# Optimization experiments

Hardware: AMD Instinct MI355X
Metric: run time of the kernel (lower is better)

## Reference

```python
import jax, jax.numpy as jnp
import numpy as np

EPS = 1e-5
TEMPERATURE = 1.0

def _finger_masks():
    # (5, 21) anatomical hyperedge masks: fingers cover node indices 1..20 in groups of 4
    m = np.zeros((5, 21), np.float32)
    for i in range(5):
        m[i, 1 + 4 * i: 5 + 4 * i] = 1.0
    return jnp.asarray(m)

def setup_inputs() -> dict:
    key = jax.random.key(0)
    ks = jax.random.split(key, 13)
    N, C, T, V, E = 128, 128, 256, 21, 8
    return {
        "x": jax.random.normal(ks[0], (N, C, T, V), jnp.float32),
        "dyn_w": jax.random.normal(ks[1], (E, C), jnp.float32) * 0.05,
        "dyn_b": jax.random.normal(ks[2], (E,), jnp.float32) * 0.05,
        "dyn_gamma": jax.random.uniform(ks[3], (E,), jnp.float32, 0.5, 1.5),
        "dyn_beta": jax.random.normal(ks[4], (E,), jnp.float32) * 0.05,
        "dyn_mean": jax.random.normal(ks[5], (E,), jnp.float32) * 0.05,
        "dyn_var": jax.random.uniform(ks[6], (E,), jnp.float32, 0.5, 1.5),
        "ft_w": jax.random.normal(ks[7], (C, C), jnp.float32) * 0.05,
        "ft_b": jax.random.normal(ks[8], (C,), jnp.float32) * 0.05,
        "ft_gamma": jax.random.uniform(ks[9], (C,), jnp.float32, 0.5, 1.5),
        "ft_beta": jax.random.normal(ks[10], (C,), jnp.float32) * 0.05,
        "ft_mean": jax.random.normal(ks[11], (C,), jnp.float32) * 0.05,
        "ft_var": jax.random.uniform(ks[12], (C,), jnp.float32, 0.5, 1.5),
    }

def reference(x, dyn_w, dyn_b, dyn_gamma, dyn_beta, dyn_mean, dyn_var,
              ft_w, ft_b, ft_gamma, ft_beta, ft_mean, ft_var):
    N = x.shape[0]
    # dynamic hyperedge generation: mean over T -> conv1x1 -> BN -> ReLU -> softmax over V
    xm = x.mean(axis=2)                                         # (N, C, V)
    h = jnp.einsum('ncv,ec->nev', xm, dyn_w) + dyn_b[None, :, None]
    scale = dyn_gamma * jax.lax.rsqrt(dyn_var + EPS)
    h = (h - dyn_mean[None, :, None]) * scale[None, :, None] + dyn_beta[None, :, None]
    h = jax.nn.relu(h)
    H_dyn = jax.nn.softmax(h / TEMPERATURE, axis=-1)            # (N, E, V)
    H_phy = jnp.broadcast_to(_finger_masks()[None], (N, 5, 21))
    H = jnp.concatenate([H_dyn, H_phy], axis=1)                 # (N, M=E+5, V)
    # feature transform: conv1x1 -> BN -> ReLU
    xf = jnp.einsum('nctv,oc->notv', x, ft_w) + ft_b[None, :, None, None]
    fscale = ft_gamma * jax.lax.rsqrt(ft_var + EPS)
    xf = (xf - ft_mean[None, :, None, None]) * fscale[None, :, None, None] + ft_beta[None, :, None, None]
    xf = jax.nn.relu(xf)                                        # (N, Cout, T, V)
    # hypergraph message passing: node -> edge -> node
    Y = jnp.einsum('nmv,nctv->ncmt', H, xf)                     # (N, Cout, M, T)
    Xr = jnp.einsum('nmv,ncmt->nctv', H, Y)                     # (N, Cout, T, V)
    return Xr + x  # residual (in_channels == out_channels)
```

## Files before the change

### kernel.cpp

```cpp
#include <hip/hip_runtime.h>
#include <hip/hip_bf16.h>
#include <math.h>

#define EPS 1e-5f

static constexpr int N_ = 128, C_ = 128, T_ = 256, V_ = 21, E_ = 8, M_ = 13;
static constexpr int TV_ = T_ * V_;
static constexpr int NT_ = 8;
static constexpr int ST_ = NT_ * V_;
static constexpr int XF_PITCH = 48;

typedef short bf16x8 __attribute__((ext_vector_type(8)));
typedef short s16x4  __attribute__((ext_vector_type(4)));
typedef float f32x4  __attribute__((ext_vector_type(4)));

__device__ inline short f2bf(float v) {
    __hip_bfloat16 b = __float2bfloat16(v);
    return *reinterpret_cast<short*>(&b);
}

__global__ __launch_bounds__(256) void prep_kernel(
    const float* __restrict__ ft_w, const float* __restrict__ ft_b,
    const float* __restrict__ ft_gamma, const float* __restrict__ ft_beta,
    const float* __restrict__ ft_mean, const float* __restrict__ ft_var,
    __hip_bfloat16* __restrict__ w_bf, float* __restrict__ sc_g, float* __restrict__ sh_g)
{
    int tid = blockIdx.x * 256 + threadIdx.x;
    if (tid < C_ * C_) w_bf[tid] = __float2bfloat16(ft_w[tid]);
    if (tid < C_) {
        float sc = ft_gamma[tid] * rsqrtf(ft_var[tid] + EPS);
        sc_g[tid] = sc;
        sh_g[tid] = (ft_b[tid] - ft_mean[tid]) * sc + ft_beta[tid];
    }
}

__global__ __launch_bounds__(256) void mean_kernel(const float* __restrict__ x,
                                                   float* __restrict__ xm) {
    __shared__ float slab[TV_];
    __shared__ float partial[V_ * 8];
    const int nc = blockIdx.x;
    const int tid = threadIdx.x;
    const float4* src4 = (const float4*)(x + (size_t)nc * TV_);
    float4* slab4 = (float4*)slab;
    #pragma unroll
    for (int it = 0; it < 6; ++it) {
        int idx = it * 256 + tid;
        if (idx < TV_ / 4) slab4[idx] = src4[idx];
    }
    __syncthreads();
    if (tid < V_ * 8) {
        int v = tid >> 3, g = tid & 7;
        float s = 0.f;
        #pragma unroll
        for (int tt = 0; tt < 32; ++tt) s += slab[(g * 32 + tt) * V_ + v];
        partial[v * 8 + g] = s;
    }
    __syncthreads();
    if (tid < V_) {
        float s = 0.f;
        #pragma unroll
        for (int g = 0; g < 8; ++g) s += partial[tid * 8 + g];
        xm[(size_t)nc * V_ + tid] = s * (1.0f / T_);
    }
}

__global__ __launch_bounds__(64) void hyper_kernel(
    const float* __restrict__ xm, const float* __restrict__ dyn_w,
    const float* __restrict__ dyn_b,
    const float* __restrict__ dyn_gamma, const float* __restrict__ dyn_beta,
    const float* __restrict__ dyn_mean, const float* __restrict__ dyn_var,
    __hip_bfloat16* __restrict__ A_bf)
{
    __shared__ float xs[C_ * V_];
    __shared__ float Hs[M_ * V_];
    const int n = blockIdx.x;
    const int l = threadIdx.x;
    const float* src = xm + (size_t)n * C_ * V_;
    for (int idx = l; idx < C_ * V_; idx += 64) xs[idx] = src[idx];
    __syncthreads();
    for (int idx = l; idx < E_ * V_; idx += 64) {
        int e = idx / V_, v = idx - e * V_;
        float acc = 0.f;
        for (int c = 0; c < C_; ++c) acc = fmaf(xs[c * V_ + v], dyn_w[e * C_ + c], acc);
        acc += dyn_b[e];
        float scale = dyn_gamma[e] * rsqrtf(dyn_var[e] + EPS);
        acc = (acc - dyn_mean[e]) * scale + dyn_beta[e];
        Hs[idx] = fmaxf(acc, 0.f);
    }
    __syncthreads();
    if (l < E_) {
        float row[V_];
        float mx = -1e30f;
        #pragma unroll
        for (int v = 0; v < V_; ++v) { row[v] = Hs[l * V_ + v]; mx = fmaxf(mx, row[v]); }
        float s = 0.f;
        #pragma unroll
        for (int v = 0; v < V_; ++v) { row[v] = __expf(row[v] - mx); s += row[v]; }
        float inv = 1.0f / s;
        #pragma unroll
        for (int v = 0; v < V_; ++v) Hs[l * V_ + v] = row[v] * inv;
    } else if (l < M_) {
        int i = l - E_;
        #pragma unroll
        for (int v = 0; v < V_; ++v)
            Hs[l * V_ + v] = (v >= 1 + 4 * i && v < 5 + 4 * i) ? 1.0f : 0.0f;
    }
    __syncthreads();
    for (int idx = l; idx < 32 * 32; idx += 64) {
        int u = idx >> 5, v = idx & 31;
        float s = 0.f;
        if (u < V_ && v < V_) {
            #pragma unroll
            for (int m = 0; m < M_; ++m) s = fmaf(Hs[m * V_ + u], Hs[m * V_ + v], s);
        }
        A_bf[(size_t)n * 1024 + idx] = __float2bfloat16(s);
    }
}

__global__ __launch_bounds__(512) void main_kernel(
    const float* __restrict__ x, const __hip_bfloat16* __restrict__ w_bf,
    const float* __restrict__ sc_g, const float* __restrict__ sh_g,
    const __hip_bfloat16* __restrict__ A_bf, float* __restrict__ out)
{
    __shared__ __align__(16) char lds[49280];
    __shared__ float sc_s[C_], sh_s[C_];

    const int st = blockIdx.x;
    const int n  = blockIdx.y;
    const int tid = threadIdx.x;
    const int w = tid >> 6;
    const int l = tid & 63;
    const int hi = l >> 4;
    const int lo = l & 15;
    const int s0 = st * ST_;
    const size_t xbase = (size_t)n * C_ * TV_ + s0;

    if (tid < C_) { sc_s[tid] = sc_g[tid]; sh_s[tid] = sh_g[tid]; }

    const int o_row = 16 * w + lo;
    bf16x8 wf[4];
    #pragma unroll
    for (int kk = 0; kk < 4; ++kk)
        wf[kk] = *(const bf16x8*)((const short*)w_bf + o_row * C_ + kk * 32 + 8 * hi);

    const short* Abf_n = (const short*)A_bf + (size_t)n * 1024;
    const bf16x8 bA0 = *(const bf16x8*)(Abf_n + lo * 32 + 8 * hi);
    const bf16x8 bA1 = *(const bf16x8*)(Abf_n + (16 + lo) * 32 + 8 * hi);

    for (int idx = tid; idx < (C_ / 4) * (ST_ / 4); idx += 512) {
        int cg = idx / (ST_ / 4), q = idx - cg * (ST_ / 4);
        int c0 = cg * 4, sq = q * 4;
        f32x4 f[4];
        #pragma unroll
        for (int i = 0; i < 4; ++i)
            f[i] = *(const f32x4*)(x + xbase + (size_t)(c0 + i) * TV_ + sq);
        #pragma unroll
        for (int i = 0; i < 4; ++i) {
            int s = sq + i;
            s16x4 pk;
            #pragma unroll
            for (int j = 0; j < 4; ++j) pk[j] = f2bf(f[j][i]);
            int byte = (s * 256 + c0 * 2) ^ ((s & 7) << 4);
            *(s16x4*)(lds + byte) = pk;
        }
    }
    if (tid < 256) {
        int s = ST_ + (tid >> 5);
        int c4 = (tid & 31) * 4;
        int byte = (s * 256 + c4 * 2) ^ ((s & 7) << 4);
        *(unsigned long long*)(lds + byte) = 0ull;
    }
    __syncthreads();

    f32x4 acc[11];
    #pragma unroll
    for (int nf = 0; nf < 11; ++nf) acc[nf] = (f32x4){0.f, 0.f, 0.f, 0.f};
    #pragma unroll
    for (int kk = 0; kk < 4; ++kk) {
        #pragma unroll
        for (int nf = 0; nf < 11; ++nf) {
            int srow = 16 * nf + lo;
            int byte = (srow * 256 + (kk * 32 + 8 * hi) * 2) ^ ((srow & 7) << 4);
            bf16x8 b = *(const bf16x8*)(lds + byte);
            acc[nf] = __builtin_amdgcn_mfma_f32_16x16x32_bf16(wf[kk], b, acc[nf], 0, 0, 0);
        }
    }
    __syncthreads();

    const int obase = 16 * w + 4 * hi;
    float scr[4], shr[4];
    #pragma unroll
    for (int r = 0; r < 4; ++r) { scr[r] = sc_s[obase + r]; shr[r] = sh_s[obase + r]; }
    #pragma unroll
    for (int nf = 0; nf < 11; ++nf) {
        int s = 16 * nf + lo;
        if (s < ST_) {
            int t = s / V_, u = s - t * V_;
            #pragma unroll
            for (int r = 0; r < 4; ++r) {
                float vv = fmaxf(fmaf(acc[nf][r], scr[r], shr[r]), 0.f);
                *(short*)(lds + ((obase + r) * 8 + t) * XF_PITCH + u * 2) = f2bf(vv);
            }
        }
    }
    for (int row = tid; row < 1024; row += 512) {
        *(short*)(lds + row * XF_PITCH + 42) = 0;
        *(int*)(lds + row * XF_PITCH + 44) = 0;
    }
    if (tid < 4) *(int*)(lds + 49152 + tid * 4) = 0;
    __syncthreads();

    bf16x8 xfr[8];
    #pragma unroll
    for (int i = 0; i < 8; ++i) {
        int row = 16 * (8 * w + i) + lo;
        xfr[i] = *(const bf16x8*)(lds + row * XF_PITCH + 16 * hi);
    }
    #pragma unroll
    for (int i = 0; i < 8; ++i) {
        f32x4 d0 = (f32x4){0.f, 0.f, 0.f, 0.f};
        f32x4 d1 = (f32x4){0.f, 0.f, 0.f, 0.f};
        d0 = __builtin_amdgcn_mfma_f32_16x16x32_bf16(xfr[i], bA0, d0, 0, 0, 0);
        d1 = __builtin_amdgcn_mfma_f32_16x16x32_bf16(xfr[i], bA1, d1, 0, 0, 0);
        int row0 = 16 * (8 * w + i) + 4 * hi;
        #pragma unroll
        for (int r = 0; r < 4; ++r) {
            int row = row0 + r;
            int o = row >> 3, t = row & 7;
            size_t g = xbase + (size_t)o * TV_ + t * V_;
            out[g + lo] = d0[r] + x[g + lo];
            if (lo < V_ - 16) out[g + 16 + lo] = d1[r] + x[g + 16 + lo];
        }
    }
}

extern "C" void kernel_launch(void* const* d_in, const int* in_sizes, int n_in,
                              void* d_out, int out_size, void* d_ws, size_t ws_size,
                              hipStream_t stream) {
    const float* x         = (const float*)d_in[0];
    const float* dyn_w     = (const float*)d_in[1];
    const float* dyn_b     = (const float*)d_in[2];
    const float* dyn_gamma = (const float*)d_in[3];
    const float* dyn_beta  = (const float*)d_in[4];
    const float* dyn_mean  = (const float*)d_in[5];
    const float* dyn_var   = (const float*)d_in[6];
    const float* ft_w      = (const float*)d_in[7];
    const float* ft_b      = (const float*)d_in[8];
    const float* ft_gamma  = (const float*)d_in[9];
    const float* ft_beta   = (const float*)d_in[10];
    const float* ft_mean   = (const float*)d_in[11];
    const float* ft_var    = (const float*)d_in[12];
    float* out = (float*)d_out;

    char* ws = (char*)d_ws;
    float* xm  = (float*)ws;                                   ws += (size_t)N_ * C_ * V_ * 4;
    __hip_bfloat16* A_bf = (__hip_bfloat16*)ws;                ws += (size_t)N_ * 1024 * 2;
    __hip_bfloat16* w_bf = (__hip_bfloat16*)ws;                ws += (size_t)C_ * C_ * 2;
    float* sc_g = (float*)ws;                                  ws += C_ * 4;
    float* sh_g = (float*)ws;                                  ws += C_ * 4;

    prep_kernel<<<64, 256, 0, stream>>>(ft_w, ft_b, ft_gamma, ft_beta, ft_mean, ft_var,
                                        w_bf, sc_g, sh_g);
    mean_kernel<<<N_ * C_, 256, 0, stream>>>(x, xm);
    hyper_kernel<<<N_, 64, 0, stream>>>(xm, dyn_w, dyn_b, dyn_gamma, dyn_beta,
                                        dyn_mean, dyn_var, A_bf);
    main_kernel<<<dim3(32, 128), 512, 0, stream>>>(x, w_bf, sc_g, sh_g, A_bf, out);
}
```

Baseline: 336.8 us.

## Pre-transpose x into bf16 MFMA fragment tiles fused with mean reduction

Adds a transpose kernel that reads x once, converts it to bf16 in MFMA-fragment order in a workspace buffer, and accumulates the T-mean with atomics. This replaces the separate mean pass over fp32 x. The main kernel then loads the pre-swizzled tiles straight into LDS with global_load_lds and takes the residual from the bf16 tile instead of re-reading fp32 x. The main kernel's second stage is split into two halves so LDS use drops and more blocks can run per CU. Trade-offs: a bf16 residual loses precision, the bf16 intermediate costs extra global writes and reads, and a sliced fallback path is used when the workspace is too small.

```diff
diff --git a/kernel.cpp b/kernel.cpp
--- a/kernel.cpp
+++ b/kernel.cpp
@@ -8,22 +8,35 @@
 static constexpr int TV_ = T_ * V_;
 static constexpr int NT_ = 8;
 static constexpr int ST_ = NT_ * V_;
-static constexpr int XF_PITCH = 48;
+static constexpr int TILE_B = 176 * 256;
+static constexpr int NCHUNK = TILE_B / 1024;
+static constexpr int SPITCH = 272;
+static constexpr int XFOFF = TILE_B;
+static constexpr int XF_BYTES = 512 * 48 + 64;
 
 typedef short bf16x8 __attribute__((ext_vector_type(8)));
 typedef short s16x4  __attribute__((ext_vector_type(4)));
 typedef float f32x4  __attribute__((ext_vector_type(4)));
 
-__device__ inline short f2bf(float v) {
-    __hip_bfloat16 b = __float2bfloat16(v);
-    return *reinterpret_cast<short*>(&b);
+__device__ inline short f2bf(float v) { __hip_bfloat16 b = __float2bfloat16(v); return *reinterpret_cast<short*>(&b); }
+__device__ inline float bf2f(short s) { __hip_bfloat16 b = *reinterpret_cast<__hip_bfloat16*>(&s); return __bfloat162float(b); }
+__device__ inline int saddr(int s, int c2) { return (s * SPITCH + c2) ^ (((s >> 2) & 7) << 4); }
+__device__ inline int fragb(int s, int c) {
+    return ((c >> 5) * 11 + (s >> 4)) * 1024 + (((c >> 3) & 3) * 16 + (s & 15)) * 16 + (c & 7) * 2;
+}
+#define EXOR(r) ((((r) >> 5) & 3) << 4)
+
+__device__ inline void gload16(const void* g, void* l) {
+    __builtin_amdgcn_global_load_lds((const __attribute__((address_space(1))) unsigned int*)g,
+                                     (__attribute__((address_space(3))) unsigned int*)l, 16, 0, 0);
 }
 
 __global__ __launch_bounds__(256) void prep_kernel(
     const float* __restrict__ ft_w, const float* __restrict__ ft_b,
     const float* __restrict__ ft_gamma, const float* __restrict__ ft_beta,
     const float* __restrict__ ft_mean, const float* __restrict__ ft_var,
-    __hip_bfloat16* __restrict__ w_bf, float* __restrict__ sc_g, float* __restrict__ sh_g)
+    __hip_bfloat16* __restrict__ w_bf, float* __restrict__ sc_g, float* __restrict__ sh_g,
+    float* __restrict__ xm)
 {
     int tid = blockIdx.x * 256 + threadIdx.x;
     if (tid < C_ * C_) w_bf[tid] = __float2bfloat16(ft_w[tid]);
@@ -32,6 +45,8 @@
         sc_g[tid] = sc;
         sh_g[tid] = (ft_b[tid] - ft_mean[tid]) * sc + ft_beta[tid];
     }
+    #pragma unroll
+    for (int j = 0; j < 21; ++j) xm[tid + 16384 * j] = 0.f;
 }
 
 __global__ __launch_bounds__(256) void mean_kernel(const float* __restrict__ x,
@@ -60,7 +75,77 @@
         float s = 0.f;
         #pragma unroll
         for (int g = 0; g < 8; ++g) s += partial[tid * 8 + g];
-        xm[(size_t)nc * V_ + tid] = s * (1.0f / T_);
+        xm[(size_t)nc * V_ + tid] = s;
+    }
+}
+
+template<bool DO_MEAN>
+__global__ __launch_bounds__(256, 4) void trans_kernel(
+    const float* __restrict__ x, int n0,
+    __hip_bfloat16* __restrict__ xt,
+    float* __restrict__ xm)
+{
+    __shared__ __align__(16) char sc[176 * SPITCH];
+    const int st = blockIdx.x;
+    const int n = n0 + blockIdx.y;
+    const int tid = threadIdx.x;
+    const size_t xn = (size_t)n * C_ * TV_;
+    const int s0 = st * ST_;
+
+    for (int r6 = 0; r6 < 6; ++r6) {
+        int idx = tid + 256 * r6;
+        if (idx < 1344) {
+            int cg = idx / 42, q = idx - cg * 42;
+            int c0 = cg * 4, sq = 4 * q;
+            f32x4 f[4];
+            #pragma unroll
+            for (int i = 0; i < 4; ++i)
+                f[i] = *(const f32x4*)(x + xn + (size_t)(c0 + i) * TV_ + s0 + sq);
+            #pragma unroll
+            for (int i2 = 0; i2 < 4; ++i2) {
+                int s = sq + i2;
+                s16x4 pk = { f2bf(f[0][i2]), f2bf(f[1][i2]), f2bf(f[2][i2]), f2bf(f[3][i2]) };
+                *(s16x4*)(sc + saddr(s, c0 * 2)) = pk;
+            }
+        }
+    }
+    if (tid < 128) {
+        int row = 168 + (tid >> 4), off = (tid & 15) * 16;
+        *(f32x4*)(sc + saddr(row, 0) + ((off ^ 0) )) = (f32x4){0.f, 0.f, 0.f, 0.f};
+    }
+    __syncthreads();
+
+    if (DO_MEAN) {
+        const int c = tid >> 1, h = tid & 1;
+        const int sb = 84 * h;
+        float vs[V_];
+        #pragma unroll
+        for (int v = 0; v < V_; ++v) vs[v] = 0.f;
+        #pragma unroll
+        for (int t4 = 0; t4 < 4; ++t4) {
+            #pragma unroll
+            for (int v = 0; v < V_; ++v) {
+                int s = sb + t4 * V_ + v;
+                vs[v] += bf2f(*(const short*)(sc + saddr(s, c * 2)));
+            }
+        }
+        #pragma unroll
+        for (int v = 0; v < V_; ++v) {
+            float tot = vs[v] + __shfl_xor(vs[v], 1);
+            if (h == 0) atomicAdd(&xm[((size_t)n * C_ + c) * V_ + v], tot);
+        }
+    }
+
+    __hip_bfloat16* dst = xt + (size_t)(blockIdx.y * 32 + st) * (TILE_B / 2);
+    const int wv = tid >> 6, l = tid & 63;
+    #pragma unroll
+    for (int k = 0; k < 11; ++k) {
+        int ch = wv * 11 + k;
+        int kk = ch / 11, nf = ch - 11 * kk;
+        int s = nf * 16 + (l & 15);
+        int c0 = kk * 32 + (l >> 4) * 8;
+        f32x4 val = *(const f32x4*)(sc + saddr(s, c0 * 2));
+        *(f32x4*)((char*)dst + ch * 1024 + l * 16) = val;
     }
 }
 
@@ -76,7 +161,7 @@
     const int n = blockIdx.x;
     const int l = threadIdx.x;
     const float* src = xm + (size_t)n * C_ * V_;
-    for (int idx = l; idx < C_ * V_; idx += 64) xs[idx] = src[idx];
+    for (int idx = l; idx < C_ * V_; idx += 64) xs[idx] = src[idx] * (1.0f / 256.0f);
     __syncthreads();
     for (int idx = l; idx < E_ * V_; idx += 64) {
         int e = idx / V_, v = idx - e * V_;
@@ -117,120 +202,108 @@
     }
 }
 
-__global__ __launch_bounds__(512) void main_kernel(
-    const float* __restrict__ x, const __hip_bfloat16* __restrict__ w_bf,
+__global__ __launch_bounds__(512, 4) void main_kernel(
+    int n0, const __hip_bfloat16* __restrict__ xt,
+    const __hip_bfloat16* __restrict__ w_bf,
     const float* __restrict__ sc_g, const float* __restrict__ sh_g,
     const __hip_bfloat16* __restrict__ A_bf, float* __restrict__ out)
 {
-    __shared__ __align__(16) char lds[49280];
-    __shared__ float sc_s[C_], sh_s[C_];
-
+    __shared__ __align__(16) char lds[TILE_B + XF_BYTES];
     const int st = blockIdx.x;
-    const int n  = blockIdx.y;
+    const int n = n0 + blockIdx.y;
     const int tid = threadIdx.x;
-    const int w = tid >> 6;
-    const int l = tid & 63;
-    const int hi = l >> 4;
-    const int lo = l & 15;
-    const int s0 = st * ST_;
-    const size_t xbase = (size_t)n * C_ * TV_ + s0;
-
-    if (tid < C_) { sc_s[tid] = sc_g[tid]; sh_s[tid] = sh_g[tid]; }
+    const int w = tid >> 6, l = tid & 63;
+    const int hi = l >> 4, lo = l & 15;
+    const int t0 = st * NT_;
+    const size_t xn = (size_t)n * C_ * TV_;
+
+    const char* tsrc = (const char*)xt + (size_t)(blockIdx.y * 32 + st) * TILE_B;
+    #pragma unroll
+    for (int k = 0; k < 6; ++k) {
+        int ch = w + 8 * k;
+        if (ch < NCHUNK) gload16(tsrc + ch * 1024 + l * 16, lds + ch * 1024);
+    }
+
+    {
+        int row = tid;
+        int e = EXOR(row);
+        *(short*)(lds + XFOFF + ((row * 48 + 42) ^ e)) = 0;
+        *(int*)(lds + XFOFF + ((row * 48 + 44) ^ e)) = 0;
+        if (tid < 4) *(f32x4*)(lds + XFOFF + 24576 + tid * 16) = (f32x4){0.f, 0.f, 0.f, 0.f};
+    }
 
     const int o_row = 16 * w + lo;
     bf16x8 wf[4];
     #pragma unroll
     for (int kk = 0; kk < 4; ++kk)
         wf[kk] = *(const bf16x8*)((const short*)w_bf + o_row * C_ + kk * 32 + 8 * hi);
-
     const short* Abf_n = (const short*)A_bf + (size_t)n * 1024;
     const bf16x8 bA0 = *(const bf16x8*)(Abf_n + lo * 32 + 8 * hi);
     const bf16x8 bA1 = *(const bf16x8*)(Abf_n + (16 + lo) * 32 + 8 * hi);
 
-    for (int idx = tid; idx < (C_ / 4) * (ST_ / 4); idx += 512) {
-        int cg = idx / (ST_ / 4), q = idx - cg * (ST_ / 4);
-        int c0 = cg * 4, sq = q * 4;
-        f32x4 f[4];
-        #pragma unroll
-        for (int i = 0; i < 4; ++i)
-            f[i] = *(const f32x4*)(x + xbase + (size_t)(c0 + i) * TV_ + sq);
-        #pragma unroll
-        for (int i = 0; i < 4; ++i) {
-            int s = sq + i;
-            s16x4 pk;
-            #pragma unroll
-            for (int j = 0; j < 4; ++j) pk[j] = f2bf(f[j][i]);
-            int byte = (s * 256 + c0 * 2) ^ ((s & 7) << 4);
-            *(s16x4*)(lds + byte) = pk;
-        }
-    }
-    if (tid < 256) {
-        int s = ST_ + (tid >> 5);
-        int c4 = (tid & 31) * 4;
-        int byte = (s * 256 + c4 * 2) ^ ((s & 7) << 4);
-        *(unsigned long long*)(lds + byte) = 0ull;
-    }
-    __syncthreads();
-
-    f32x4 acc[11];
-    #pragma unroll
-    for (int nf = 0; nf < 11; ++nf) acc[nf] = (f32x4){0.f, 0.f, 0.f, 0.f};
-    #pragma unroll
-    for (int kk = 0; kk < 4; ++kk) {
-        #pragma unroll
-        for (int nf = 0; nf < 11; ++nf) {
-            int srow = 16 * nf + lo;
-            int byte = (srow * 256 + (kk * 32 + 8 * hi) * 2) ^ ((srow & 7) << 4);
-            bf16x8 b = *(const bf16x8*)(lds + byte);
-            acc[nf] = __builtin_amdgcn_mfma_f32_16x16x32_bf16(wf[kk], b, acc[nf], 0, 0, 0);
-        }
-    }
-    __syncthreads();
-
     const int obase = 16 * w + 4 * hi;
     float scr[4], shr[4];
     #pragma unroll
-    for (int r = 0; r < 4; ++r) { scr[r] = sc_s[obase + r]; shr[r] = sh_s[obase + r]; }
-    #pragma unroll
-    for (int nf = 0; nf < 11; ++nf) {
-        int s = 16 * nf + lo;
-        if (s < ST_) {
-            int t = s / V_, u = s - t * V_;
+    for (int r = 0; r < 4; ++r) { scr[r] = sc_g[obase + r]; shr[r] = sh_g[obase + r]; }
+
+    __syncthreads();
+
+    f32x4 acc[11];
+    #pragma unroll
+    for (int nf = 0; nf < 11; ++nf) acc[nf] = (f32x4){0.f, 0.f, 0.f, 0.f};
+    #pragma unroll
+    for (int kk = 0; kk < 4; ++kk) {
+        #pragma unroll
+        for (int nf = 0; nf < 11; ++nf) {
+            bf16x8 b = *(const bf16x8*)(lds + (kk * 11 + nf) * 1024 + l * 16);
+            acc[nf] = __builtin_amdgcn_mfma_f32_16x16x32_bf16(wf[kk], b, acc[nf], 0, 0, 0);
+        }
+    }
+
+    #pragma unroll
+    for (int half = 0; half < 2; ++half) {
+        if ((w >> 2) == half) {
+            #pragma unroll
+            for (int nf = 0; nf < 11; ++nf) {
+                int s = 16 * nf + lo;
+                if (s < ST_) {
+                    int t = s / V_, u = s - t * V_;
+                    #pragma unroll
+                    for (int r = 0; r < 4; ++r) {
+                        float vv = fmaxf(fmaf(acc[nf][r], scr[r], shr[r]), 0.f);
+                        int lr = ((obase & 63) + r) * NT_ + t;
+                        *(short*)(lds + XFOFF + ((lr * 48 + u * 2) ^ EXOR(lr))) = f2bf(vv);
+                    }
+                }
+            }
+        }
+        __syncthreads();
+
+        bf16x8 xfr[4];
+        #pragma unroll
+        for (int i = 0; i < 4; ++i) {
+            int lr = 16 * (4 * w + i) + lo;
+            xfr[i] = *(const bf16x8*)(lds + XFOFF + ((lr * 48 + 16 * hi) ^ EXOR(lr)));
+        }
+        #pragma unroll
+        for (int i = 0; i < 4; ++i) {
+            f32x4 d0 = (f32x4){0.f, 0.f, 0.f, 0.f};
+            f32x4 d1 = (f32x4){0.f, 0.f, 0.f, 0.f};
+            d0 = __builtin_amdgcn_mfma_f32_16x16x32_bf16(xfr[i], bA0, d0, 0, 0, 0);
+            d1 = __builtin_amdgcn_mfma_f32_16x16x32_bf16(xfr[i], bA1, d1, 0, 0, 0);
+            int row0 = 16 * (4 * w + i) + 4 * hi;
             #pragma unroll
             for (int r = 0; r < 4; ++r) {
-                float vv = fmaxf(fmaf(acc[nf][r], scr[r], shr[r]), 0.f);
-                *(short*)(lds + ((obase + r) * 8 + t) * XF_PITCH + u * 2) = f2bf(vv);
+                int grow = half * 512 + row0 + r;
+                int o = grow >> 3, tl = grow & 7;
+                size_t g = xn + (size_t)o * TV_ + (size_t)(t0 + tl) * V_;
+                int s1 = tl * V_ + lo;
+                out[g + lo] = d0[r] + bf2f(*(const short*)(lds + fragb(s1, o)));
+                if (lo < V_ - 16)
+                    out[g + 16 + lo] = d1[r] + bf2f(*(const short*)(lds + fragb(s1 + 16, o)));
             }
         }
-    }
-    for (int row = tid; row < 1024; row += 512) {
-        *(short*)(lds + row * XF_PITCH + 42) = 0;
-        *(int*)(lds + row * XF_PITCH + 44) = 0;
-    }
-    if (tid < 4) *(int*)(lds + 49152 + tid * 4) = 0;
-    __syncthreads();
-
-    bf16x8 xfr[8];
-    #pragma unroll
-    for (int i = 0; i < 8; ++i) {
-        int row = 16 * (8 * w + i) + lo;
-        xfr[i] = *(const bf16x8*)(lds + row * XF_PITCH + 16 * hi);
-    }
-    #pragma unroll
-    for (int i = 0; i < 8; ++i) {
-        f32x4 d0 = (f32x4){0.f, 0.f, 0.f, 0.f};
-        f32x4 d1 = (f32x4){0.f, 0.f, 0.f, 0.f};
-        d0 = __builtin_amdgcn_mfma_f32_16x16x32_bf16(xfr[i], bA0, d0, 0, 0, 0);
-        d1 = __builtin_amdgcn_mfma_f32_16x16x32_bf16(xfr[i], bA1, d1, 0, 0, 0);
-        int row0 = 16 * (8 * w + i) + 4 * hi;
-        #pragma unroll
-        for (int r = 0; r < 4; ++r) {
-            int row = row0 + r;
-            int o = row >> 3, t = row & 7;
-            size_t g = xbase + (size_t)o * TV_ + t * V_;
-            out[g + lo] = d0[r] + x[g + lo];
-            if (lo < V_ - 16) out[g + 16 + lo] = d1[r] + x[g + 16 + lo];
-        }
+        if (half == 0) __syncthreads();
     }
 }
 
@@ -253,16 +326,34 @@
     float* out = (float*)d_out;
 
     char* ws = (char*)d_ws;
-    float* xm  = (float*)ws;                                   ws += (size_t)N_ * C_ * V_ * 4;
-    __hip_bfloat16* A_bf = (__hip_bfloat16*)ws;                ws += (size_t)N_ * 1024 * 2;
-    __hip_bfloat16* w_bf = (__hip_bfloat16*)ws;                ws += (size_t)C_ * C_ * 2;
-    float* sc_g = (float*)ws;                                  ws += C_ * 4;
-    float* sh_g = (float*)ws;                                  ws += C_ * 4;
+    float* xm  = (float*)ws;                     ws += (size_t)N_ * C_ * V_ * 4;
+    __hip_bfloat16* A_bf = (__hip_bfloat16*)ws;  ws += (size_t)N_ * 1024 * 2;
+    __hip_bfloat16* w_bf = (__hip_bfloat16*)ws;  ws += (size_t)C_ * C_ * 2;
+    float* sc_g = (float*)ws;                    ws += C_ * 4;
+    float* sh_g = (float*)ws;                    ws += C_ * 4;
+    __hip_bfloat16* xt = (__hip_bfloat16*)ws;
+    size_t fixed = (size_t)(ws - (char*)d_ws);
+    size_t xt_full = (size_t)N_ * 32 * TILE_B;
 
     prep_kernel<<<64, 256, 0, stream>>>(ft_w, ft_b, ft_gamma, ft_beta, ft_mean, ft_var,
-                                        w_bf, sc_g, sh_g);
-    mean_kernel<<<N_ * C_, 256, 0, stream>>>(x, xm);
-    hyper_kernel<<<N_, 64, 0, stream>>>(xm, dyn_w, dyn_b, dyn_gamma, dyn_beta,
-                                        dyn_mean, dyn_var, A_bf);
-    main_kernel<<<dim3(32, 128), 512, 0, stream>>>(x, w_bf, sc_g, sh_g, A_bf, out);
-}
+                                        w_bf, sc_g, sh_g, xm);
+
+    if (ws_size >= fixed + xt_full) {
+        trans_kernel<true><<<dim3(32, N_), 256, 0, stream>>>(x, 0, xt, xm);
+        hyper_kernel<<<N_, 64, 0, stream>>>(xm, dyn_w, dyn_b, dyn_gamma, dyn_beta,
+                                            dyn_mean, dyn_var, A_bf);
+        main_kernel<<<dim3(32, N_), 512, 0, stream>>>(0, xt, w_bf, sc_g, sh_g, A_bf, out);
+    } else {
+        mean_kernel<<<N_ * C_, 256, 0, stream>>>(x, xm);
+        hyper_kernel<<<N_, 64, 0, stream>>>(xm, dyn_w, dyn_b, dyn_gamma, dyn_beta,
+                                            dyn_mean, dyn_var, A_bf);
+        const int NSL = 16;
+        size_t sliceShorts = (size_t)NSL * 32 * (TILE_B / 2);
+        for (int sl = 0; sl < N_ / NSL; ++sl) {
+            __hip_bfloat16* xts = xt + (sl & 1) * sliceShorts;
+            trans_kernel<false><<<dim3(32, NSL), 256, 0, stream>>>(x, sl * NSL, xts, xm);
+            main_kernel<<<dim3(32, NSL), 512, 0, stream>>>(sl * NSL, xts, w_bf, sc_g, sh_g,
+                                                           A_bf, out);
+        }
+    }
+}
```

New measurement: 728.3 us. +116.3%, slower.

## Convert x to bf16 once in mean pass and stage main kernel from bf16 copy

Applied to the files above, without the earlier changes.

The mean kernel now also writes a bf16 copy of x, and the main kernel stages its GEMM input and residual from that half-width copy instead of fp32 x. It also changes the LDS swizzles for the staged tile and the xf buffer to reduce bank conflicts. This aims to cut main-kernel global read bytes and the in-kernel conversion work. It adds an extra bf16 write pass and makes the residual use bf16-rounded x, which lowers output accuracy.

```diff
diff --git a/kernel.cpp b/kernel.cpp
--- a/kernel.cpp
+++ b/kernel.cpp
@@ -10,6 +10,9 @@
 static constexpr int ST_ = NT_ * V_;
 static constexpr int XF_PITCH = 48;
 
+#define SWZ(s)  (((((s) >> 3) & 15) ^ ((((s) & 7)) << 1)) << 4)
+#define EXOR(r) ((((r) >> 5) & 3) << 4)
+
 typedef short bf16x8 __attribute__((ext_vector_type(8)));
 typedef short s16x4  __attribute__((ext_vector_type(4)));
 typedef float f32x4  __attribute__((ext_vector_type(4)));
@@ -17,6 +20,10 @@
 __device__ inline short f2bf(float v) {
     __hip_bfloat16 b = __float2bfloat16(v);
     return *reinterpret_cast<short*>(&b);
+}
+__device__ inline float bf2f_u(unsigned short s) {
+    __hip_bfloat16 b = *reinterpret_cast<__hip_bfloat16*>(&s);
+    return __bfloat162float(b);
 }
 
 __global__ __launch_bounds__(256) void prep_kernel(
@@ -34,18 +41,27 @@
     }
 }
 
-__global__ __launch_bounds__(256) void mean_kernel(const float* __restrict__ x,
-                                                   float* __restrict__ xm) {
+__global__ __launch_bounds__(256) void cvt_kernel(const float* __restrict__ x,
+                                                  __hip_bfloat16* __restrict__ xbf,
+                                                  float* __restrict__ xm) {
     __shared__ float slab[TV_];
     __shared__ float partial[V_ * 8];
     const int nc = blockIdx.x;
     const int tid = threadIdx.x;
-    const float4* src4 = (const float4*)(x + (size_t)nc * TV_);
-    float4* slab4 = (float4*)slab;
-    #pragma unroll
-    for (int it = 0; it < 6; ++it) {
-        int idx = it * 256 + tid;
-        if (idx < TV_ / 4) slab4[idx] = src4[idx];
+    const f32x4* src4 = (const f32x4*)(x + (size_t)nc * TV_);
+    f32x4* slab4 = (f32x4*)slab;
+    short* dst = (short*)xbf + (size_t)nc * TV_;
+
+    #pragma unroll
+    for (int it = 0; it < 3; ++it) {
+        int p = it * 256 + tid;
+        if (p < 672) {
+            f32x4 a = src4[2 * p], b = src4[2 * p + 1];
+            slab4[2 * p] = a; slab4[2 * p + 1] = b;
+            bf16x8 pk = { f2bf(a[0]), f2bf(a[1]), f2bf(a[2]), f2bf(a[3]),
+                          f2bf(b[0]), f2bf(b[1]), f2bf(b[2]), f2bf(b[3]) };
+            *(bf16x8*)(dst + 8 * p) = pk;
+        }
     }
     __syncthreads();
     if (tid < V_ * 8) {
@@ -118,7 +134,7 @@
 }
 
 __global__ __launch_bounds__(512) void main_kernel(
-    const float* __restrict__ x, const __hip_bfloat16* __restrict__ w_bf,
+    const __hip_bfloat16* __restrict__ xbf, const __hip_bfloat16* __restrict__ w_bf,
     const float* __restrict__ sc_g, const float* __restrict__ sh_g,
     const __hip_bfloat16* __restrict__ A_bf, float* __restrict__ out)
 {
@@ -133,7 +149,8 @@
     const int hi = l >> 4;
     const int lo = l & 15;
     const int s0 = st * ST_;
-    const size_t xbase = (size_t)n * C_ * TV_ + s0;
+    const unsigned short* xr = (const unsigned short*)xbf + (size_t)n * C_ * TV_;
+    float* ob = out + (size_t)n * C_ * TV_;
 
     if (tid < C_) { sc_s[tid] = sc_g[tid]; sh_s[tid] = sh_g[tid]; }
 
@@ -143,33 +160,28 @@
     for (int kk = 0; kk < 4; ++kk)
         wf[kk] = *(const bf16x8*)((const short*)w_bf + o_row * C_ + kk * 32 + 8 * hi);
 
-    const short* Abf_n = (const short*)A_bf + (size_t)n * 1024;
-    const bf16x8 bA0 = *(const bf16x8*)(Abf_n + lo * 32 + 8 * hi);
-    const bf16x8 bA1 = *(const bf16x8*)(Abf_n + (16 + lo) * 32 + 8 * hi);
-
-    for (int idx = tid; idx < (C_ / 4) * (ST_ / 4); idx += 512) {
-        int cg = idx / (ST_ / 4), q = idx - cg * (ST_ / 4);
-        int c0 = cg * 4, sq = q * 4;
-        f32x4 f[4];
-        #pragma unroll
-        for (int i = 0; i < 4; ++i)
-            f[i] = *(const f32x4*)(x + xbase + (size_t)(c0 + i) * TV_ + sq);
-        #pragma unroll
-        for (int i = 0; i < 4; ++i) {
-            int s = sq + i;
-            s16x4 pk;
-            #pragma unroll
-            for (int j = 0; j < 4; ++j) pk[j] = f2bf(f[j][i]);
-            int byte = (s * 256 + c0 * 2) ^ ((s & 7) << 4);
-            *(s16x4*)(lds + byte) = pk;
-        }
-    }
-    if (tid < 256) {
-        int s = ST_ + (tid >> 5);
-        int c4 = (tid & 31) * 4;
-        int byte = (s * 256 + c4 * 2) ^ ((s & 7) << 4);
-        *(unsigned long long*)(lds + byte) = 0ull;
-    }
+    const short* An = (const short*)A_bf + n * 1024;
+    const bf16x8 bA0 = *(const bf16x8*)(An + lo * 32 + 8 * hi);
+    const bf16x8 bA1 = *(const bf16x8*)(An + (16 + lo) * 32 + 8 * hi);
+
+    auto stage_item = [&](int idx) {
+        int cg = idx / 21, q = idx - 21 * cg;
+        int c0 = 4 * cg, sb = 8 * q;
+        const unsigned short* p = xr + c0 * TV_ + s0 + sb;
+        bf16x8 r0 = *(const bf16x8*)(p);
+        bf16x8 r1 = *(const bf16x8*)(p + TV_);
+        bf16x8 r2 = *(const bf16x8*)(p + 2 * TV_);
+        bf16x8 r3 = *(const bf16x8*)(p + 3 * TV_);
+        #pragma unroll
+        for (int si = 0; si < 8; ++si) {
+            int s = sb + si;
+            s16x4 pk = { r0[si], r1[si], r2[si], r3[si] };
+            *(s16x4*)(lds + ((s * 256 + 8 * cg) ^ SWZ(s))) = pk;
+        }
+    };
+    stage_item(tid);
+    if (tid < 672 - 512) stage_item(tid + 512);
+    if (tid < 128) *(f32x4*)(lds + 168 * 256 + 16 * tid) = (f32x4){0.f, 0.f, 0.f, 0.f};
     __syncthreads();
 
     f32x4 acc[11];
@@ -180,8 +192,7 @@
         #pragma unroll
         for (int nf = 0; nf < 11; ++nf) {
             int srow = 16 * nf + lo;
-            int byte = (srow * 256 + (kk * 32 + 8 * hi) * 2) ^ ((srow & 7) << 4);
-            bf16x8 b = *(const bf16x8*)(lds + byte);
+            bf16x8 b = *(const bf16x8*)(lds + ((srow * 256 + (kk * 32 + 8 * hi) * 2) ^ SWZ(srow)));
             acc[nf] = __builtin_amdgcn_mfma_f32_16x16x32_bf16(wf[kk], b, acc[nf], 0, 0, 0);
         }
     }
@@ -199,22 +210,27 @@
             #pragma unroll
             for (int r = 0; r < 4; ++r) {
                 float vv = fmaxf(fmaf(acc[nf][r], scr[r], shr[r]), 0.f);
-                *(short*)(lds + ((obase + r) * 8 + t) * XF_PITCH + u * 2) = f2bf(vv);
+                int row = (obase + r) * NT_ + t;
+                *(short*)(lds + ((row * XF_PITCH + 2 * u) ^ EXOR(row))) = f2bf(vv);
             }
         }
     }
-    for (int row = tid; row < 1024; row += 512) {
-        *(short*)(lds + row * XF_PITCH + 42) = 0;
-        *(int*)(lds + row * XF_PITCH + 44) = 0;
-    }
-    if (tid < 4) *(int*)(lds + 49152 + tid * 4) = 0;
+    {
+        int row = tid;
+        *(short*)(lds + ((row * XF_PITCH + 42) ^ EXOR(row))) = 0;
+        *(int*)(lds + ((row * XF_PITCH + 44) ^ EXOR(row))) = 0;
+        row = tid + 512;
+        *(short*)(lds + ((row * XF_PITCH + 42) ^ EXOR(row))) = 0;
+        *(int*)(lds + ((row * XF_PITCH + 44) ^ EXOR(row))) = 0;
+    }
+    if (tid < 8) *(f32x4*)(lds + 49152 + 16 * tid) = (f32x4){0.f, 0.f, 0.f, 0.f};
     __syncthreads();
 
     bf16x8 xfr[8];
     #pragma unroll
     for (int i = 0; i < 8; ++i) {
-        int row = 16 * (8 * w + i) + lo;
-        xfr[i] = *(const bf16x8*)(lds + row * XF_PITCH + 16 * hi);
+        int lr = 16 * (8 * w + i) + lo;
+        xfr[i] = *(const bf16x8*)(lds + ((lr * XF_PITCH + 16 * hi) ^ EXOR(lr)));
     }
     #pragma unroll
     for (int i = 0; i < 8; ++i) {
@@ -226,10 +242,10 @@
         #pragma unroll
         for (int r = 0; r < 4; ++r) {
             int row = row0 + r;
-            int o = row >> 3, t = row & 7;
-            size_t g = xbase + (size_t)o * TV_ + t * V_;
-            out[g + lo] = d0[r] + x[g + lo];
-            if (lo < V_ - 16) out[g + 16 + lo] = d1[r] + x[g + 16 + lo];
+            int o = row >> 3, tl = row & 7;
+            int g = o * TV_ + s0 + tl * V_;
+            ob[g + lo] = d0[r] + bf2f_u(xr[g + lo]);
+            if (lo < V_ - 16) ob[g + 16 + lo] = d1[r] + bf2f_u(xr[g + 16 + lo]);
         }
     }
 }
@@ -253,16 +269,17 @@
     float* out = (float*)d_out;
 
     char* ws = (char*)d_ws;
-    float* xm  = (float*)ws;                                   ws += (size_t)N_ * C_ * V_ * 4;
-    __hip_bfloat16* A_bf = (__hip_bfloat16*)ws;                ws += (size_t)N_ * 1024 * 2;
-    __hip_bfloat16* w_bf = (__hip_bfloat16*)ws;                ws += (size_t)C_ * C_ * 2;
-    float* sc_g = (float*)ws;                                  ws += C_ * 4;
-    float* sh_g = (float*)ws;                                  ws += C_ * 4;
+    float* xm  = (float*)ws;                     ws += (size_t)N_ * C_ * V_ * 4;
+    __hip_bfloat16* A_bf = (__hip_bfloat16*)ws;  ws += (size_t)N_ * 1024 * 2;
+    __hip_bfloat16* w_bf = (__hip_bfloat16*)ws;  ws += (size_t)C_ * C_ * 2;
+    float* sc_g = (float*)ws;                    ws += C_ * 4;
+    float* sh_g = (float*)ws;                    ws += C_ * 4;
+    __hip_bfloat16* xbf = (__hip_bfloat16*)ws;
 
     prep_kernel<<<64, 256, 0, stream>>>(ft_w, ft_b, ft_gamma, ft_beta, ft_mean, ft_var,
                                         w_bf, sc_g, sh_g);
-    mean_kernel<<<N_ * C_, 256, 0, stream>>>(x, xm);
+    cvt_kernel<<<N_ * C_, 256, 0, stream>>>(x, xbf, xm);
     hyper_kernel<<<N_, 64, 0, stream>>>(xm, dyn_w, dyn_b, dyn_gamma, dyn_beta,
                                         dyn_mean, dyn_var, A_bf);
-    main_kernel<<<dim3(32, 128), 512, 0, stream>>>(x, w_bf, sc_g, sh_g, A_bf, out);
-}
+    main_kernel<<<dim3(32, 128), 512, 0, stream>>>(xbf, w_bf, sc_g, sh_g, A_bf, out);
+}
```

Result: no change. 341.9 us (+1.5%).
